# Kernel optimization log

Measured on AMD Instinct MI355X. Metric: run time of the kernel, lower is better.

The kernel has to match this reference:

```python
import jax, jax.numpy as jnp
import numpy as np

T, B, E, H = 200, 2048, 256, 512
P0, P1, NC = 256, 128, 1
ALPHA = 0.3  # keras LeakyReLU default


def _predict(h, W0, b0, W1, b1, Wf, bf):
    # Dense -> LeakyReLU -> (dropout=identity) x2, then sigmoid(Dense)
    h = jax.nn.leaky_relu(h @ W0 + b0, ALPHA)
    h = jax.nn.leaky_relu(h @ W1 + b1, ALPHA)
    return jax.nn.sigmoid(h @ Wf + bf)  # [B, 1]


def setup_inputs() -> dict:
    key = jax.random.key(0)
    ks = jax.random.split(key, 24)
    s = 0.05  # keras 'random_normal' initializer stddev
    d = {
        "inputs": jax.random.normal(ks[0], (T, B, E), jnp.float32),
        # gate order along leading axis: f, i, o, g
        "Wx_c": s * jax.random.normal(ks[1], (4, E, H), jnp.float32),
        "bx_c": jnp.zeros((4, H), jnp.float32),
        "Wh_c": s * jax.random.normal(ks[2], (4, H, H), jnp.float32),
        "Wx_v": s * jax.random.normal(ks[3], (4, E, H), jnp.float32),
        "bx_v": jnp.zeros((4, H), jnp.float32),
        "Wh_v": s * jax.random.normal(ks[4], (4, H, H), jnp.float32),
        # order: s_c_hat_c, s_c_hat_v, s_v_hat_v, s_v_hat_c
        "Ws": s * jax.random.normal(ks[5], (4, H, H), jnp.float32),
        "Wpc0": s * jax.random.normal(ks[6], (H, P0), jnp.float32),
        "bpc0": jnp.zeros((P0,), jnp.float32),
        "Wpc1": s * jax.random.normal(ks[7], (P0, P1), jnp.float32),
        "bpc1": jnp.zeros((P1,), jnp.float32),
        "Wfcc": s * jax.random.normal(ks[8], (P1, NC), jnp.float32),
        "bfcc": jnp.zeros((NC,), jnp.float32),
        "Wpv0": s * jax.random.normal(ks[9], (H, P0), jnp.float32),
        "bpv0": jnp.zeros((P0,), jnp.float32),
        "Wpv1": s * jax.random.normal(ks[10], (P0, P1), jnp.float32),
        "bpv1": jnp.zeros((P1,), jnp.float32),
        "Wfcv": s * jax.random.normal(ks[11], (P1, NC), jnp.float32),
        "bfcv": jnp.zeros((NC,), jnp.float32),
    }
    return d


def reference(inputs, Wx_c, bx_c, Wh_c, Wx_v, bx_v, Wh_v, Ws,
              Wpc0, bpc0, Wpc1, bpc1, Wfcc, bfcc,
              Wpv0, bpv0, Wpv1, bpv1, Wfcv, bfcv):
    batch = inputs.shape[1]
    zeros = jnp.zeros((batch, H), inputs.dtype)
    # initial g = predict_c(H_c=0), broadcast in place of tf.tile(g,[1,n_hidden])
    g0 = _predict(zeros, Wpc0, bpc0, Wpc1, bpc1, Wfcc, bfcc)  # [B,1]
    ones1 = jnp.ones_like(g0)

    def step(carry, x):
        H_c, H_v, s_c, s_v, g, pc, pv = carry
        # click stream gates: f,i,o,g fused along leading axis
        gx = jnp.einsum('be,keh->kbh', x, Wx_c) + bx_c[:, None, :]
        gh = jnp.einsum('bh,khg->kbg', H_c, Wh_c)
        pre = gx + gh
        f_c, i_c, o_c = jax.nn.sigmoid(pre[0]), jax.nn.sigmoid(pre[1]), jax.nn.sigmoid(pre[2])
        g_c = jnp.tanh(pre[3])
        s_c_hat = jnp.tanh((1.0 - g) * (H_c @ Ws[0]) + g * (H_v @ Ws[1]))
        s_c = s_c_hat + i_c * g_c + (1.0 - g) * (f_c * s_c)
        H_c = o_c * jnp.tanh(s_c)
        H_c_p = _predict(H_c, Wpc0, bpc0, Wpc1, bpc1, Wfcc, bfcc)  # [B,1]
        # no click_label branch: g = H_c_p
        g = H_c_p
        pc = jnp.where(H_c_p >= 0.5, ones1, (1.0 - H_c_p) * pc)
        # conversion stream gates (driven by updated H_c)
        gxv = jnp.einsum('be,keh->kbh', x, Wx_v) + bx_v[:, None, :]
        ghv = jnp.einsum('bh,khg->kbg', H_c, Wh_v)
        prev = gxv + ghv
        f_v, i_v, o_v = jax.nn.sigmoid(prev[0]), jax.nn.sigmoid(prev[1]), jax.nn.sigmoid(prev[2])
        g_v = jnp.tanh(prev[3])
        s_v_hat = jnp.tanh(H_v @ Ws[2] + g * (H_c @ Ws[3]))
        s_v = s_v_hat + (1.0 - g) * s_v + g * (f_v * s_v + i_v * g_v)
        H_v = (1.0 - g) * H_v + g * (o_v * jnp.tanh(s_v))
        H_v_p = _predict(H_v, Wpv0, bpv0, Wpv1, bpv1, Wfcv, bfcv) * H_c_p
        pv = jnp.where(H_c_p >= 0.5, ones1, (1.0 - H_v_p) * pv)
        return (H_c, H_v, s_c, s_v, g, pc, pv), (H_c_p, H_v_p)

    carry0 = (zeros, zeros, zeros, zeros, g0, ones1, ones1)
    _, (pred_c, pred_v) = jax.lax.scan(step, carry0, inputs)
    return pred_c, pred_v  # each [T, B, 1]
```

## Files before the change

kernel.cpp:

```cpp
#include <hip/hip_runtime.h>
#include <cstdint>
#include <cstddef>

constexpr int T_STEPS = 200;
constexpr int BATCH   = 2048;
constexpr int E_DIM   = 256;
constexpr int H_DIM   = 512;
constexpr int P0_DIM  = 256;
constexpr int P1_DIM  = 128;
constexpr float ALPHA = 0.3f;

typedef __attribute__((ext_vector_type(8))) _Float16 f16x8;
typedef __attribute__((ext_vector_type(4))) float f32x4;

__device__ __forceinline__ float sigmoidf_(float x){ return 1.0f/(1.0f+expf(-x)); }

__device__ __forceinline__ unsigned short f2h(float f){
    union { _Float16 h; unsigned short u; } v;
    v.h = (_Float16)f;
    return v.u;
}

#define GLOAD16(gp, lp) __builtin_amdgcn_global_load_lds( \
    (const __attribute__((address_space(1))) unsigned int*)(gp), \
    (__attribute__((address_space(3))) unsigned int*)(lp), 16, 0, 0)

template<int ROWS>
__device__ __forceinline__ void stage64(const unsigned short* __restrict__ src, int ldk,
                                        char* ldsbase){
    constexpr int TOT = ROWS * 8;
    const int tid = threadIdx.x;
#pragma unroll
    for (int i = 0; i < TOT/256; ++i){
        const int gsl = i*256 + tid;
        const int r = gsl >> 3, s = gsl & 7;
        const int ksrc = ((s ^ (r & 7)) << 3);
        GLOAD16(src + (size_t)r*ldk + ksrc, ldsbase + gsl*16);
    }
}

__device__ __forceinline__ f16x8 ldsfragh(const char* ldsbase, int row, int kslot){
    return *(const f16x8*)(ldsbase + row*128 + ((kslot ^ (row & 7)) << 4));
}

__device__ __forceinline__ void mm_loop128h(
    const unsigned short* __restrict__ A, int lda,
    const unsigned short* __restrict__ B, int ldb,
    int K, f32x4 (&acc)[4][4], char* lds, int wr, int wc, int lr, int lq)
{
    stage64<128>(A, lda, lds);
    stage64<128>(B, ldb, lds + 16384);
    int cur = 0;
    for (int k0 = 0; k0 < K; k0 += 64){
        char* bufc = lds + cur*32768;
        if (k0 + 64 < K){
            char* bufn = lds + (cur^1)*32768;
            stage64<128>(A + k0 + 64, lda, bufn);
            stage64<128>(B + k0 + 64, ldb, bufn + 16384);
            asm volatile("s_waitcnt vmcnt(8)" ::: "memory");
        } else {
            asm volatile("s_waitcnt vmcnt(0)" ::: "memory");
        }
        __builtin_amdgcn_s_barrier();
        __builtin_amdgcn_sched_barrier(0);
        __builtin_amdgcn_s_setprio(1);
#pragma unroll
        for (int kk = 0; kk < 2; ++kk){
            f16x8 a[4], b[4];
#pragma unroll
            for (int m = 0; m < 4; ++m) a[m] = ldsfragh(bufc, wr*64 + m*16 + lr, kk*4 + lq);
#pragma unroll
            for (int n = 0; n < 4; ++n) b[n] = ldsfragh(bufc + 16384, wc*64 + n*16 + lr, kk*4 + lq);
#pragma unroll
            for (int m = 0; m < 4; ++m)
#pragma unroll
                for (int n = 0; n < 4; ++n)
                    acc[m][n] = __builtin_amdgcn_mfma_f32_16x16x32_f16(a[m], b[n], acc[m][n], 0,0,0);
        }
        __builtin_amdgcn_s_setprio(0);
        __builtin_amdgcn_sched_barrier(0);
        __builtin_amdgcn_s_barrier();
        cur ^= 1;
    }
}

__device__ __forceinline__ void gates_tile(
    int id,
    const unsigned short* __restrict__ Xh,
    const unsigned short* __restrict__ Hh,
    const unsigned short* __restrict__ WT,
    const float* __restrict__ bias, float* __restrict__ gates,
    char* lds, int wr, int wc, int lr, int lq)
{
    const int sw = ((id & 7) << 5) + (id >> 3);
    const int brow = (sw & 15) * 128;
    const int bcol = (sw >> 4) * 128;

    f32x4 acc[4][4];
#pragma unroll
    for (int m = 0; m < 4; ++m)
#pragma unroll
        for (int n = 0; n < 4; ++n){ f32x4 z = {0.f,0.f,0.f,0.f}; acc[m][n] = z; }

    mm_loop128h(Xh + (size_t)brow*E_DIM, E_DIM,
                WT + (size_t)bcol*768, 768,
                E_DIM, acc, lds, wr, wc, lr, lq);
    mm_loop128h(Hh + (size_t)brow*H_DIM, H_DIM,
                WT + (size_t)bcol*768 + E_DIM, 768,
                H_DIM, acc, lds, wr, wc, lr, lq);

    const int z = bcol >> 9;
    const int hbase = (bcol & 511) + wc*64;
    float* gz = gates + (size_t)z * BATCH * H_DIM;
#pragma unroll
    for (int m = 0; m < 4; ++m){
#pragma unroll
        for (int n = 0; n < 4; ++n){
            const int h = hbase + n*16 + lr;
            const float bs = bias[z*H_DIM + h];
#pragma unroll
            for (int r = 0; r < 4; ++r){
                const int b2 = brow + wr*64 + m*16 + lq*4 + r;
                float v = acc[m][n][r] + bs;
                v = (z < 3) ? sigmoidf_(v) : tanhf(v);
                gz[(size_t)b2 * H_DIM + h] = v;
            }
        }
    }
}

__device__ __forceinline__ void comb_tile(
    int jid,
    const unsigned short* __restrict__ A,
    const unsigned short* __restrict__ B,
    float* __restrict__ outp, char* lds, int wr, int wc, int lr, int lq)
{
    const int brow = (jid >> 2) * 128, bcol = (jid & 3) * 128;
    f32x4 acc[4][4];
#pragma unroll
    for (int m = 0; m < 4; ++m)
#pragma unroll
        for (int n = 0; n < 4; ++n){ f32x4 z = {0.f,0.f,0.f,0.f}; acc[m][n] = z; }

    mm_loop128h(A + (size_t)brow*H_DIM, H_DIM,
                B + (size_t)bcol*H_DIM, H_DIM,
                H_DIM, acc, lds, wr, wc, lr, lq);
#pragma unroll
    for (int m = 0; m < 4; ++m){
#pragma unroll
        for (int n = 0; n < 4; ++n){
            const int h = bcol + wc*64 + n*16 + lr;
#pragma unroll
            for (int r = 0; r < 4; ++r){
                const int b2 = brow + wr*64 + m*16 + lq*4 + r;
                outp[(size_t)b2 * H_DIM + h] = acc[m][n][r];
            }
        }
    }
}

__device__ __forceinline__ void predict_dev(
    int pblk, const unsigned short* __restrict__ Hh,
    const unsigned short* __restrict__ W0T, const float* __restrict__ b0,
    const unsigned short* __restrict__ W1T, const float* __restrict__ b1,
    const float* __restrict__ Wf, const float* __restrict__ bf_,
    float* gstate, const float* __restrict__ gmul, float* pred, char* lds)
{
    char*  ldsA = lds;
    char*  ldsB = lds + 4096;
    char*  ldsP = lds + 36864;
    float* sums = (float*)(lds + 53248);
    const int tid = threadIdx.x, lane = tid & 63, w = tid >> 6;
    const int lr = lane & 15, lq = lane >> 4;
    const int brow = pblk * 32;

    f32x4 acc0[2][4];
#pragma unroll
    for (int m = 0; m < 2; ++m)
#pragma unroll
        for (int n = 0; n < 4; ++n){ f32x4 z = {0.f,0.f,0.f,0.f}; acc0[m][n] = z; }

    for (int k0 = 0; k0 < H_DIM; k0 += 64){
        stage64<32>(Hh + (size_t)brow*H_DIM + k0, H_DIM, ldsA);
        stage64<256>(W0T + k0, H_DIM, ldsB);
        __syncthreads();
#pragma unroll
        for (int kk = 0; kk < 2; ++kk){
            f16x8 a[2], b[4];
#pragma unroll
            for (int m = 0; m < 2; ++m) a[m] = ldsfragh(ldsA, m*16 + lr, kk*4 + lq);
#pragma unroll
            for (int n = 0; n < 4; ++n) b[n] = ldsfragh(ldsB, w*64 + n*16 + lr, kk*4 + lq);
#pragma unroll
            for (int m = 0; m < 2; ++m)
#pragma unroll
                for (int n = 0; n < 4; ++n)
                    acc0[m][n] = __builtin_amdgcn_mfma_f32_16x16x32_f16(a[m], b[n], acc0[m][n], 0,0,0);
        }
        __syncthreads();
    }
#pragma unroll
    for (int m = 0; m < 2; ++m){
#pragma unroll
        for (int n = 0; n < 4; ++n){
            const int col = w*64 + n*16 + lr;
            const float bs = b0[col];
#pragma unroll
            for (int r = 0; r < 4; ++r){
                const int row = m*16 + lq*4 + r;
                float x = acc0[m][n][r] + bs;
                x = (x > 0.0f) ? x : ALPHA*x;
                *(unsigned short*)(ldsP + row*512 + ((((col >> 3)) ^ (row & 7)) << 4) + (col & 7)*2) = f2h(x);
            }
        }
    }
    __syncthreads();

    f32x4 accp[2][2];
#pragma unroll
    for (int m = 0; m < 2; ++m)
#pragma unroll
        for (int n = 0; n < 2; ++n){ f32x4 z = {0.f,0.f,0.f,0.f}; accp[m][n] = z; }

    for (int k0 = 0; k0 < P0_DIM; k0 += 64){
        stage64<128>(W1T + k0, P0_DIM, ldsB);
        __syncthreads();
#pragma unroll
        for (int kk = 0; kk < 2; ++kk){
            f16x8 a[2], b[2];
#pragma unroll
            for (int m = 0; m < 2; ++m){
                const int row = m*16 + lr;
                const int slot = (k0 >> 3) + kk*4 + lq;
                a[m] = *(const f16x8*)(ldsP + row*512 + ((slot ^ (row & 7)) << 4));
            }
#pragma unroll
            for (int n = 0; n < 2; ++n) b[n] = ldsfragh(ldsB, w*32 + n*16 + lr, kk*4 + lq);
#pragma unroll
            for (int m = 0; m < 2; ++m)
#pragma unroll
                for (int n = 0; n < 2; ++n)
                    accp[m][n] = __builtin_amdgcn_mfma_f32_16x16x32_f16(a[m], b[n], accp[m][n], 0,0,0);
        }
        __syncthreads();
    }

    float part[8];
#pragma unroll
    for (int j = 0; j < 8; ++j) part[j] = 0.0f;
#pragma unroll
    for (int m = 0; m < 2; ++m){
#pragma unroll
        for (int n = 0; n < 2; ++n){
            const int col = w*32 + n*16 + lr;
            const float bs = b1[col], wf = Wf[col];
#pragma unroll
            for (int r = 0; r < 4; ++r){
                float x = accp[m][n][r] + bs;
                x = (x > 0.0f) ? x : ALPHA*x;
                part[m*4 + r] += x * wf;
            }
        }
    }
#pragma unroll
    for (int mask = 1; mask < 16; mask <<= 1)
#pragma unroll
        for (int j = 0; j < 8; ++j) part[j] += __shfl_xor(part[j], mask);
    if (lr == 0){
#pragma unroll
        for (int j = 0; j < 8; ++j){
            const int row = (j >> 2)*16 + lq*4 + (j & 3);
            sums[w*32 + row] = part[j];
        }
    }
    __syncthreads();
    if (tid < 32){
        float tot = sums[tid] + sums[32 + tid] + sums[64 + tid] + sums[96 + tid] + bf_[0];
        float val = sigmoidf_(tot);
        const int rowg = brow + tid;
        if (gmul)   val *= gmul[rowg];
        if (gstate) gstate[rowg] = val;
        if (pred)   pred[rowg]   = val;
    }
}

__device__ __forceinline__ void xcvt_dev(int blk, const float* __restrict__ x,
                                         unsigned short* __restrict__ oh)
{
    const int tid = threadIdx.x;
#pragma unroll
    for (int j = 0; j < 4; ++j){
        const int t = blk*256 + tid + j*32768;
        float4 v = ((const float4*)x)[t];
        ushort4 h;
        h.x = f2h(v.x); h.y = f2h(v.y); h.z = f2h(v.z); h.w = f2h(v.w);
        ((ushort4*)oh)[t] = h;
    }
}

__global__ __launch_bounds__(256, 2) void k_mmA(
    const unsigned short* __restrict__ Xh,
    const unsigned short* __restrict__ Hc, const unsigned short* __restrict__ Hv,
    const unsigned short* __restrict__ WT,
    const float* __restrict__ bias, float* __restrict__ gates,
    const unsigned short* __restrict__ Ws0, float* __restrict__ a1,
    const unsigned short* __restrict__ Ws1, float* __restrict__ a2,
    const unsigned short* __restrict__ Ws2, float* __restrict__ a1v,
    const unsigned short* __restrict__ W0Tv, const float* __restrict__ b0v,
    const unsigned short* __restrict__ W1Tv, const float* __restrict__ b1v,
    const float* __restrict__ Wfv, const float* __restrict__ bfv,
    const float* __restrict__ g, float* __restrict__ predv)
{
    __shared__ __align__(16) char lds[65536];
    const int tid = threadIdx.x;
    const int lane = tid & 63, wid = tid >> 6;
    const int wr = wid >> 1, wc = wid & 1;
    const int lr = lane & 15, lq = lane >> 4;
    const int id = blockIdx.x;

    if (id < 256){
        gates_tile(id, Xh, Hc, WT, bias, gates, lds, wr, wc, lr, lq);
    } else if (id < 448){
        const int j = (id - 256) >> 6, jid = (id - 256) & 63;
        if (j == 0)      comb_tile(jid, Hc, Ws0, a1,  lds, wr, wc, lr, lq);
        else if (j == 1) comb_tile(jid, Hv, Ws1, a2,  lds, wr, wc, lr, lq);
        else             comb_tile(jid, Hv, Ws2, a1v, lds, wr, wc, lr, lq);
    } else {
        predict_dev(id - 448, Hv, W0Tv, b0v, W1Tv, b1v, Wfv, bfv,
                    nullptr, g, predv, lds);
    }
}

__global__ __launch_bounds__(256, 2) void k_mmB(
    const unsigned short* __restrict__ Xh,
    const unsigned short* __restrict__ Hc,
    const unsigned short* __restrict__ WT,
    const float* __restrict__ bias, float* __restrict__ gates,
    const unsigned short* __restrict__ Ws3, float* __restrict__ a2v,
    const unsigned short* __restrict__ W0Tc, const float* __restrict__ b0c,
    const unsigned short* __restrict__ W1Tc, const float* __restrict__ b1c,
    const float* __restrict__ Wfc, const float* __restrict__ bfc,
    float* __restrict__ g, float* __restrict__ predc,
    const float* __restrict__ xnext, unsigned short* __restrict__ Xnh)
{
    __shared__ __align__(16) char lds[65536];
    const int tid = threadIdx.x;
    const int lane = tid & 63, wid = tid >> 6;
    const int wr = wid >> 1, wc = wid & 1;
    const int lr = lane & 15, lq = lane >> 4;
    const int id = blockIdx.x;

    if (id < 256){
        gates_tile(id, Xh, Hc, WT, bias, gates, lds, wr, wc, lr, lq);
    } else if (id < 320){
        comb_tile(id - 256, Hc, Ws3, a2v, lds, wr, wc, lr, lq);
    } else if (id < 384){
        predict_dev(id - 320, Hc, W0Tc, b0c, W1Tc, b1c, Wfc, bfc,
                    g, nullptr, predc, lds);
    } else {
        xcvt_dev(id - 384, xnext, Xnh);
    }
}

__global__ __launch_bounds__(256) void k_cell(
    const int mode, const float* __restrict__ gates, const float* __restrict__ a1,
    const float* __restrict__ a2, const float* __restrict__ g,
    float* __restrict__ sstate, float* __restrict__ Hv32,
    unsigned short* __restrict__ Outh)
{
    const size_t BH = (size_t)BATCH * H_DIM;
    const int i4 = blockIdx.x*256 + threadIdx.x;
    const size_t base = (size_t)i4 * 4;
    const int row = (int)(base >> 9);
    const float gv = g[row];
    union U4 { float4 v; float s[4]; };
    U4 f_, i_, o_, q_, u1, u2, sv, hv;
    f_.v = *(const float4*)&gates[base];
    i_.v = *(const float4*)&gates[BH + base];
    o_.v = *(const float4*)&gates[2*BH + base];
    q_.v = *(const float4*)&gates[3*BH + base];
    u1.v = *(const float4*)&a1[base];
    u2.v = *(const float4*)&a2[base];
    sv.v = *(const float4*)&sstate[base];
    if (mode == 1) hv.v = *(const float4*)&Hv32[base];
    U4 sn, hnew;
    union { unsigned short u[4]; ushort4 v; } hh;
#pragma unroll
    for (int e = 0; e < 4; ++e){
        float hval, s;
        if (mode == 0){
            const float shat = tanhf((1.0f - gv)*u1.s[e] + gv*u2.s[e]);
            s = shat + i_.s[e]*q_.s[e] + (1.0f - gv)*(f_.s[e]*sv.s[e]);
            hval = o_.s[e] * tanhf(s);
        } else {
            const float shat = tanhf(u1.s[e] + gv*u2.s[e]);
            const float svo = sv.s[e];
            s = shat + (1.0f - gv)*svo + gv*(f_.s[e]*svo + i_.s[e]*q_.s[e]);
            hval = (1.0f - gv)*hv.s[e] + gv*(o_.s[e]*tanhf(s));
            hnew.s[e] = hval;
        }
        sn.s[e] = s;
        hh.u[e] = f2h(hval);
    }
    *(float4*)&sstate[base] = sn.v;
    if (mode == 1) *(float4*)&Hv32[base] = hnew.v;
    *(ushort4*)&Outh[base] = hh.v;
}

__global__ __launch_bounds__(256) void k_predict_g(
    const unsigned short* __restrict__ Hh,
    const unsigned short* __restrict__ W0T, const float* __restrict__ b0,
    const unsigned short* __restrict__ W1T, const float* __restrict__ b1,
    const float* __restrict__ Wf, const float* __restrict__ bf_,
    float* gstate, const float* __restrict__ gmul, float* pred)
{
    __shared__ __align__(16) char lds[53760];
    predict_dev(blockIdx.x, Hh, W0T, b0, W1T, b1, Wf, bf_, gstate, gmul, pred, lds);
}

__global__ __launch_bounds__(256) void k_xcvt_g(const float* __restrict__ x,
                                                unsigned short* __restrict__ oh)
{
    xcvt_dev(blockIdx.x, x, oh);
}

__global__ __launch_bounds__(256) void k_wcat(const float* __restrict__ Wx,
                                              const float* __restrict__ Wh,
                                              unsigned short* __restrict__ oh){
    const int n = blockIdx.y;
    const int k = blockIdx.x*256 + threadIdx.x;
    const int z = n >> 9, h = n & 511;
    float v = (k < 256) ? Wx[((size_t)z*E_DIM + k)*H_DIM + h]
                        : Wh[((size_t)z*H_DIM + (k - 256))*H_DIM + h];
    oh[(size_t)n*768 + k] = f2h(v);
}

__global__ __launch_bounds__(256) void k_trans(const float* __restrict__ in,
                                               unsigned short* __restrict__ oh,
                                               int K, int N){
    const int k = blockIdx.x*256 + threadIdx.x;
    const int n = blockIdx.y;
    if (k < K) oh[(size_t)n*K + k] = f2h(in[(size_t)k*N + n]);
}

__global__ __launch_bounds__(256) void k_init(float* __restrict__ sc, float* __restrict__ sv,
                                              float* __restrict__ hv32,
                                              unsigned short* __restrict__ hc0,
                                              unsigned short* __restrict__ hv0){
    const int i = blockIdx.x*256 + threadIdx.x;
    sc[i] = 0.0f; sv[i] = 0.0f; hv32[i] = 0.0f;
    hc0[i] = 0; hv0[i] = 0;
}

extern "C" void kernel_launch(void* const* d_in, const int* in_sizes, int n_in,
                              void* d_out, int out_size, void* d_ws, size_t ws_size,
                              hipStream_t stream)
{
    (void)in_sizes; (void)n_in; (void)out_size; (void)ws_size;

    const float* inputs = (const float*)d_in[0];
    const float* Wx_c   = (const float*)d_in[1];
    const float* bx_c   = (const float*)d_in[2];
    const float* Wh_c   = (const float*)d_in[3];
    const float* Wx_v   = (const float*)d_in[4];
    const float* bx_v   = (const float*)d_in[5];
    const float* Wh_v   = (const float*)d_in[6];
    const float* Ws     = (const float*)d_in[7];
    const float* Wpc0   = (const float*)d_in[8];
    const float* bpc0   = (const float*)d_in[9];
    const float* Wpc1   = (const float*)d_in[10];
    const float* bpc1   = (const float*)d_in[11];
    const float* Wfcc   = (const float*)d_in[12];
    const float* bfcc   = (const float*)d_in[13];
    const float* Wpv0   = (const float*)d_in[14];
    const float* bpv0   = (const float*)d_in[15];
    const float* Wpv1   = (const float*)d_in[16];
    const float* bpv1   = (const float*)d_in[17];
    const float* Wfcv   = (const float*)d_in[18];
    const float* bfcv   = (const float*)d_in[19];
    float* out = (float*)d_out;

    char* ws = (char*)d_ws;
    size_t off = 0;
    auto allocB = [&](size_t bytes) -> char* {
        char* p = ws + off;
        off = (off + bytes + 255) & ~(size_t)255;
        return p;
    };
    const size_t BH = (size_t)BATCH * H_DIM;
    const size_t BE = (size_t)BATCH * E_DIM;

    unsigned short* Xh[2];
    Xh[0] = (unsigned short*)allocB(BE*2);
    Xh[1] = (unsigned short*)allocB(BE*2);
    unsigned short* WcTc  = (unsigned short*)allocB((size_t)2048*768*2);
    unsigned short* WcTv  = (unsigned short*)allocB((size_t)2048*768*2);
    unsigned short* WsT   = (unsigned short*)allocB((size_t)4*H_DIM*H_DIM*2);
    unsigned short* Wp0Tc = (unsigned short*)allocB((size_t)P0_DIM*H_DIM*2);
    unsigned short* Wp0Tv = (unsigned short*)allocB((size_t)P0_DIM*H_DIM*2);
    unsigned short* Wp1Tc = (unsigned short*)allocB((size_t)P1_DIM*P0_DIM*2);
    unsigned short* Wp1Tv = (unsigned short*)allocB((size_t)P1_DIM*P0_DIM*2);
    unsigned short* Hc    = (unsigned short*)allocB(BH*2);
    unsigned short* Hv    = (unsigned short*)allocB(BH*2);
    float* sc    = (float*)allocB(BH*4);
    float* sv    = (float*)allocB(BH*4);
    float* hv32  = (float*)allocB(BH*4);
    float* gates = (float*)allocB(4*BH*4);
    float* a1    = (float*)allocB(BH*4);
    float* a2    = (float*)allocB(BH*4);
    float* a1v   = (float*)allocB(BH*4);
    float* a2v   = (float*)allocB(BH*4);
    float* g     = (float*)allocB(BATCH*4);

    const dim3 thr(256);
    const size_t HH = (size_t)H_DIM * H_DIM;

    k_wcat<<<dim3(3, 2048), thr, 0, stream>>>(Wx_c, Wh_c, WcTc);
    k_wcat<<<dim3(3, 2048), thr, 0, stream>>>(Wx_v, Wh_v, WcTv);
    for (int i = 0; i < 4; ++i)
        k_trans<<<dim3(2, 512), thr, 0, stream>>>(Ws + i*HH, WsT + i*HH, H_DIM, H_DIM);
    k_trans<<<dim3(2, 256), thr, 0, stream>>>(Wpc0, Wp0Tc, H_DIM, P0_DIM);
    k_trans<<<dim3(2, 256), thr, 0, stream>>>(Wpv0, Wp0Tv, H_DIM, P0_DIM);
    k_trans<<<dim3(1, 128), thr, 0, stream>>>(Wpc1, Wp1Tc, P0_DIM, P1_DIM);
    k_trans<<<dim3(1, 128), thr, 0, stream>>>(Wpv1, Wp1Tv, P0_DIM, P1_DIM);

    k_init<<<4096, thr, 0, stream>>>(sc, sv, hv32, Hc, Hv);
    k_predict_g<<<64, thr, 0, stream>>>(Hc, Wp0Tc, bpc0, Wp1Tc, bpc1, Wfcc, bfcc,
                                        g, nullptr, nullptr);
    k_xcvt_g<<<128, thr, 0, stream>>>(inputs, Xh[0]);

    for (int t = 0; t < T_STEPS; ++t){
        const int xs = t & 1, xn = xs ^ 1;

        const int gridA = (t > 0) ? 512 : 448;
        k_mmA<<<gridA, thr, 0, stream>>>(Xh[xs], Hc, Hv,
                                         WcTc, bx_c, gates,
                                         WsT + 0*HH, a1,
                                         WsT + 1*HH, a2,
                                         WsT + 2*HH, a1v,
                                         Wp0Tv, bpv0, Wp1Tv, bpv1, Wfcv, bfcv,
                                         g, out + (size_t)(T_STEPS + t - 1)*BATCH);
        k_cell<<<1024, thr, 0, stream>>>(0, gates, a1, a2, g, sc, nullptr, Hc);

        const int gridB = (t + 1 < T_STEPS) ? 512 : 384;
        k_mmB<<<gridB, thr, 0, stream>>>(Xh[xs], Hc,
                                         WcTv, bx_v, gates,
                                         WsT + 3*HH, a2v,
                                         Wp0Tc, bpc0, Wp1Tc, bpc1, Wfcc, bfcc,
                                         g, out + (size_t)t*BATCH,
                                         inputs + (size_t)(t+1)*BE, Xh[xn]);
        k_cell<<<1024, thr, 0, stream>>>(1, gates, a1v, a2v, g, sv, hv32, Hv);
    }
    k_predict_g<<<64, thr, 0, stream>>>(Hv, Wp0Tv, bpv0, Wp1Tv, bpv1, Wfcv, bfcv,
                                        nullptr, g, out + (size_t)(2*T_STEPS - 1)*BATCH);
}
```

Baseline: 12.02 ms.

## Fuse gate GEMMs, Ws combos and cell update into one per-stream kernel

Replaces the separate gate GEMM, Ws combination GEMMs and elementwise cell kernels with a single fused kernel. Each block computes all four gates for a 64-row by 32-hidden slice together with both Ws projections, then applies the cell update straight from LDS. Weights are reordered so that one tile holds every gate for the same hidden units, and the H and g buffers are double-buffered. This removes the large fp32 round-trips for gates and a1/a2 and cuts launches per step from four to three. The trade-offs are a smaller MMA tile (64x128) with lower reuse, and moving the predictor and input conversion into a separate launch.

```diff
diff --git a/kernel.cpp b/kernel.cpp
--- a/kernel.cpp
+++ b/kernel.cpp
@@ -43,21 +43,31 @@
     return *(const f16x8*)(ldsbase + row*128 + ((kslot ^ (row & 7)) << 4));
 }
 
-__device__ __forceinline__ void mm_loop128h(
+template<bool HAS_B1, bool HAS_B2, int KSLABS>
+__device__ __forceinline__ void fused_phase(
     const unsigned short* __restrict__ A, int lda,
-    const unsigned short* __restrict__ B, int ldb,
-    int K, f32x4 (&acc)[4][4], char* lds, int wr, int wc, int lr, int lq)
-{
-    stage64<128>(A, lda, lds);
-    stage64<128>(B, ldb, lds + 16384);
+    const unsigned short* __restrict__ B1,
+    const unsigned short* __restrict__ B2,
+    f32x4 (&accg)[2][4], f32x4 (&acce)[2],
+    char* lds, int wr, int wc, int lr, int lq)
+{
+    stage64<64>(A, lda, lds);
+    if (HAS_B1) stage64<128>(B1, 768, lds + 8192);
+    if (HAS_B2) stage64<32>(B2, 512, lds + 24576);
     int cur = 0;
-    for (int k0 = 0; k0 < K; k0 += 64){
+    for (int s = 0; s < KSLABS; ++s){
         char* bufc = lds + cur*32768;
-        if (k0 + 64 < K){
+        if (s + 1 < KSLABS){
             char* bufn = lds + (cur^1)*32768;
-            stage64<128>(A + k0 + 64, lda, bufn);
-            stage64<128>(B + k0 + 64, ldb, bufn + 16384);
-            asm volatile("s_waitcnt vmcnt(8)" ::: "memory");
+            stage64<64>(A + (s+1)*64, lda, bufn);
+            if (HAS_B1) stage64<128>(B1 + (s+1)*64, 768, bufn + 8192);
+            if (HAS_B2) stage64<32>(B2 + (s+1)*64, 512, bufn + 24576);
+            if constexpr (HAS_B1 && HAS_B2)
+                asm volatile("s_waitcnt vmcnt(7)" ::: "memory");
+            else if constexpr (HAS_B1)
+                asm volatile("s_waitcnt vmcnt(6)" ::: "memory");
+            else
+                asm volatile("s_waitcnt vmcnt(3)" ::: "memory");
         } else {
             asm volatile("s_waitcnt vmcnt(0)" ::: "memory");
         }
@@ -66,16 +76,24 @@
         __builtin_amdgcn_s_setprio(1);
 #pragma unroll
         for (int kk = 0; kk < 2; ++kk){
-            f16x8 a[4], b[4];
-#pragma unroll
-            for (int m = 0; m < 4; ++m) a[m] = ldsfragh(bufc, wr*64 + m*16 + lr, kk*4 + lq);
-#pragma unroll
-            for (int n = 0; n < 4; ++n) b[n] = ldsfragh(bufc + 16384, wc*64 + n*16 + lr, kk*4 + lq);
-#pragma unroll
-            for (int m = 0; m < 4; ++m)
-#pragma unroll
-                for (int n = 0; n < 4; ++n)
-                    acc[m][n] = __builtin_amdgcn_mfma_f32_16x16x32_f16(a[m], b[n], acc[m][n], 0,0,0);
+            f16x8 a[2];
+#pragma unroll
+            for (int m = 0; m < 2; ++m) a[m] = ldsfragh(bufc, wr*32 + m*16 + lr, kk*4 + lq);
+            if (HAS_B1){
+#pragma unroll
+                for (int n = 0; n < 4; ++n){
+                    f16x8 b = ldsfragh(bufc + 8192, wc*64 + n*16 + lr, kk*4 + lq);
+#pragma unroll
+                    for (int m = 0; m < 2; ++m)
+                        accg[m][n] = __builtin_amdgcn_mfma_f32_16x16x32_f16(a[m], b, accg[m][n], 0,0,0);
+                }
+            }
+            if (HAS_B2){
+                f16x8 b = ldsfragh(bufc + 24576, wc*16 + lr, kk*4 + lq);
+#pragma unroll
+                for (int m = 0; m < 2; ++m)
+                    acce[m] = __builtin_amdgcn_mfma_f32_16x16x32_f16(a[m], b, acce[m], 0,0,0);
+            }
         }
         __builtin_amdgcn_s_setprio(0);
         __builtin_amdgcn_sched_barrier(0);
@@ -84,79 +102,129 @@
     }
 }
 
-__device__ __forceinline__ void gates_tile(
-    int id,
+__global__ __launch_bounds__(256, 2) void k_fused(
     const unsigned short* __restrict__ Xh,
-    const unsigned short* __restrict__ Hh,
-    const unsigned short* __restrict__ WT,
-    const float* __restrict__ bias, float* __restrict__ gates,
-    char* lds, int wr, int wc, int lr, int lq)
-{
-    const int sw = ((id & 7) << 5) + (id >> 3);
-    const int brow = (sw & 15) * 128;
-    const int bcol = (sw >> 4) * 128;
-
-    f32x4 acc[4][4];
-#pragma unroll
-    for (int m = 0; m < 4; ++m)
-#pragma unroll
-        for (int n = 0; n < 4; ++n){ f32x4 z = {0.f,0.f,0.f,0.f}; acc[m][n] = z; }
-
-    mm_loop128h(Xh + (size_t)brow*E_DIM, E_DIM,
-                WT + (size_t)bcol*768, 768,
-                E_DIM, acc, lds, wr, wc, lr, lq);
-    mm_loop128h(Hh + (size_t)brow*H_DIM, H_DIM,
-                WT + (size_t)bcol*768 + E_DIM, 768,
-                H_DIM, acc, lds, wr, wc, lr, lq);
-
-    const int z = bcol >> 9;
-    const int hbase = (bcol & 511) + wc*64;
-    float* gz = gates + (size_t)z * BATCH * H_DIM;
-#pragma unroll
-    for (int m = 0; m < 4; ++m){
+    const unsigned short* __restrict__ AH,
+    const unsigned short* __restrict__ AV,
+    const unsigned short* __restrict__ WT2,
+    const float* __restrict__ bias,
+    const unsigned short* __restrict__ WsH,
+    const unsigned short* __restrict__ WsV,
+    const float* __restrict__ g,
+    float* __restrict__ sstate, float* __restrict__ Hv32,
+    unsigned short* __restrict__ Hnew,
+    const int mode)
+{
+    __shared__ __align__(16) char lds[65536];
+    const int tid = threadIdx.x;
+    const int lane = tid & 63, wid = tid >> 6;
+    const int wr = wid >> 1, wc = wid & 1;
+    const int lr = lane & 15, lq = lane >> 4;
+
+    const int id = blockIdx.x;
+    const int virt = ((id & 7) << 6) | (id >> 3);
+    const int hgrp = virt >> 5;
+    const int brow = (virt & 31) * 64;
+    const int h0   = hgrp * 32;
+
+    f32x4 accg[2][4], acceH[2], acceV[2];
+#pragma unroll
+    for (int m = 0; m < 2; ++m){
+        f32x4 z = {0.f,0.f,0.f,0.f};
+#pragma unroll
+        for (int n = 0; n < 4; ++n) accg[m][n] = z;
+        acceH[m] = z; acceV[m] = z;
+    }
+
+    const unsigned short* WTp = WT2 + (size_t)hgrp*128*768;
+    fused_phase<true,false,4>(Xh + (size_t)brow*E_DIM, E_DIM, WTp, nullptr,
+                              accg, acceH, lds, wr, wc, lr, lq);
+    fused_phase<true,true,8>(AH + (size_t)brow*H_DIM, H_DIM, WTp + E_DIM,
+                             WsH + (size_t)h0*H_DIM,
+                             accg, acceH, lds, wr, wc, lr, lq);
+    fused_phase<false,true,8>(AV + (size_t)brow*H_DIM, H_DIM, nullptr,
+                              WsV + (size_t)h0*H_DIM,
+                              accg, acceV, lds, wr, wc, lr, lq);
+
+    float* ldsG  = (float*)lds;
+    float* ldsEH = (float*)(lds + 33792);
+    float* ldsEV = (float*)(lds + 42240);
+#pragma unroll
+    for (int m = 0; m < 2; ++m){
 #pragma unroll
         for (int n = 0; n < 4; ++n){
-            const int h = hbase + n*16 + lr;
-            const float bs = bias[z*H_DIM + h];
+            const int col = wc*64 + n*16 + lr;
+            const int z = col >> 5, hl = col & 31;
+            const float bs = bias[z*H_DIM + h0 + hl];
 #pragma unroll
             for (int r = 0; r < 4; ++r){
-                const int b2 = brow + wr*64 + m*16 + lq*4 + r;
-                float v = acc[m][n][r] + bs;
+                const int row = wr*32 + m*16 + lq*4 + r;
+                float v = accg[m][n][r] + bs;
                 v = (z < 3) ? sigmoidf_(v) : tanhf(v);
-                gz[(size_t)b2 * H_DIM + h] = v;
+                ldsG[row*132 + col] = v;
             }
         }
     }
-}
-
-__device__ __forceinline__ void comb_tile(
-    int jid,
-    const unsigned short* __restrict__ A,
-    const unsigned short* __restrict__ B,
-    float* __restrict__ outp, char* lds, int wr, int wc, int lr, int lq)
-{
-    const int brow = (jid >> 2) * 128, bcol = (jid & 3) * 128;
-    f32x4 acc[4][4];
-#pragma unroll
-    for (int m = 0; m < 4; ++m)
-#pragma unroll
-        for (int n = 0; n < 4; ++n){ f32x4 z = {0.f,0.f,0.f,0.f}; acc[m][n] = z; }
-
-    mm_loop128h(A + (size_t)brow*H_DIM, H_DIM,
-                B + (size_t)bcol*H_DIM, H_DIM,
-                H_DIM, acc, lds, wr, wc, lr, lq);
-#pragma unroll
-    for (int m = 0; m < 4; ++m){
-#pragma unroll
-        for (int n = 0; n < 4; ++n){
-            const int h = bcol + wc*64 + n*16 + lr;
-#pragma unroll
-            for (int r = 0; r < 4; ++r){
-                const int b2 = brow + wr*64 + m*16 + lq*4 + r;
-                outp[(size_t)b2 * H_DIM + h] = acc[m][n][r];
-            }
-        }
-    }
+#pragma unroll
+    for (int m = 0; m < 2; ++m){
+        const int col = wc*16 + lr;
+#pragma unroll
+        for (int r = 0; r < 4; ++r){
+            const int row = wr*32 + m*16 + lq*4 + r;
+            ldsEH[row*33 + col] = acceH[m][r];
+            ldsEV[row*33 + col] = acceV[m][r];
+        }
+    }
+    __syncthreads();
+
+    const int crow = tid >> 2, ch = (tid & 3) * 8;
+    const int grow = brow + crow;
+    const float gv = g[grow];
+    const size_t gbase = (size_t)grow*H_DIM + h0 + ch;
+    union U4 { float4 v; float s[4]; };
+    U4 sv0, sv1, hv0, hv1;
+    sv0.v = *(const float4*)&sstate[gbase];
+    sv1.v = *(const float4*)&sstate[gbase + 4];
+    if (mode == 1){
+        hv0.v = *(const float4*)&Hv32[gbase];
+        hv1.v = *(const float4*)&Hv32[gbase + 4];
+    }
+    U4 sn0, sn1, hn0, hn1;
+    union { unsigned short u[8]; f16x8 v; } hh;
+#pragma unroll
+    for (int e = 0; e < 8; ++e){
+        const int hc = ch + e;
+        const float f_ = ldsG[crow*132 + hc];
+        const float i_ = ldsG[crow*132 + 32 + hc];
+        const float o_ = ldsG[crow*132 + 64 + hc];
+        const float q_ = ldsG[crow*132 + 96 + hc];
+        const float eh = ldsEH[crow*33 + hc];
+        const float ev = ldsEV[crow*33 + hc];
+        const float a1 = (mode == 0) ? eh : ev;
+        const float a2 = (mode == 0) ? ev : eh;
+        const float svo = (e < 4) ? sv0.s[e] : sv1.s[e-4];
+        float s, hval;
+        if (mode == 0){
+            const float shat = tanhf((1.0f - gv)*a1 + gv*a2);
+            s = shat + i_*q_ + (1.0f - gv)*(f_*svo);
+            hval = o_ * tanhf(s);
+        } else {
+            const float shat = tanhf(a1 + gv*a2);
+            s = shat + (1.0f - gv)*svo + gv*(f_*svo + i_*q_);
+            const float hvo = (e < 4) ? hv0.s[e] : hv1.s[e-4];
+            hval = (1.0f - gv)*hvo + gv*(o_*tanhf(s));
+            if (e < 4) hn0.s[e] = hval; else hn1.s[e-4] = hval;
+        }
+        if (e < 4) sn0.s[e] = s; else sn1.s[e-4] = s;
+        hh.u[e] = f2h(hval);
+    }
+    *(float4*)&sstate[gbase]     = sn0.v;
+    *(float4*)&sstate[gbase + 4] = sn1.v;
+    if (mode == 1){
+        *(float4*)&Hv32[gbase]     = hn0.v;
+        *(float4*)&Hv32[gbase + 4] = hn1.v;
+    }
+    *(f16x8*)&Hnew[gbase] = hh.v;
 }
 
 __device__ __forceinline__ void predict_dev(
@@ -298,113 +366,30 @@
     }
 }
 
-__global__ __launch_bounds__(256, 2) void k_mmA(
-    const unsigned short* __restrict__ Xh,
-    const unsigned short* __restrict__ Hc, const unsigned short* __restrict__ Hv,
-    const unsigned short* __restrict__ WT,
-    const float* __restrict__ bias, float* __restrict__ gates,
-    const unsigned short* __restrict__ Ws0, float* __restrict__ a1,
-    const unsigned short* __restrict__ Ws1, float* __restrict__ a2,
-    const unsigned short* __restrict__ Ws2, float* __restrict__ a1v,
-    const unsigned short* __restrict__ W0Tv, const float* __restrict__ b0v,
-    const unsigned short* __restrict__ W1Tv, const float* __restrict__ b1v,
-    const float* __restrict__ Wfv, const float* __restrict__ bfv,
-    const float* __restrict__ g, float* __restrict__ predv)
-{
-    __shared__ __align__(16) char lds[65536];
-    const int tid = threadIdx.x;
-    const int lane = tid & 63, wid = tid >> 6;
-    const int wr = wid >> 1, wc = wid & 1;
-    const int lr = lane & 15, lq = lane >> 4;
+__global__ __launch_bounds__(256) void k_LB(
+    const unsigned short* __restrict__ Hcn,
+    const unsigned short* __restrict__ Wp0Tc, const float* __restrict__ bpc0,
+    const unsigned short* __restrict__ Wp1Tc, const float* __restrict__ bpc1,
+    const float* __restrict__ Wfcc, const float* __restrict__ bfcc,
+    float* __restrict__ gnew, float* __restrict__ predc,
+    const unsigned short* __restrict__ Hvb,
+    const unsigned short* __restrict__ Wp0Tv, const float* __restrict__ bpv0,
+    const unsigned short* __restrict__ Wp1Tv, const float* __restrict__ bpv1,
+    const float* __restrict__ Wfcv, const float* __restrict__ bfcv,
+    const float* __restrict__ gold, float* __restrict__ predv,
+    const float* __restrict__ xnext, unsigned short* __restrict__ Xnh)
+{
+    __shared__ __align__(16) char lds[53760];
     const int id = blockIdx.x;
-
-    if (id < 256){
-        gates_tile(id, Xh, Hc, WT, bias, gates, lds, wr, wc, lr, lq);
-    } else if (id < 448){
-        const int j = (id - 256) >> 6, jid = (id - 256) & 63;
-        if (j == 0)      comb_tile(jid, Hc, Ws0, a1,  lds, wr, wc, lr, lq);
-        else if (j == 1) comb_tile(jid, Hv, Ws1, a2,  lds, wr, wc, lr, lq);
-        else             comb_tile(jid, Hv, Ws2, a1v, lds, wr, wc, lr, lq);
+    if (id < 64){
+        predict_dev(id, Hcn, Wp0Tc, bpc0, Wp1Tc, bpc1, Wfcc, bfcc,
+                    gnew, nullptr, predc, lds);
+    } else if (id < 128){
+        if (predv) predict_dev(id - 64, Hvb, Wp0Tv, bpv0, Wp1Tv, bpv1, Wfcv, bfcv,
+                               nullptr, gold, predv, lds);
     } else {
-        predict_dev(id - 448, Hv, W0Tv, b0v, W1Tv, b1v, Wfv, bfv,
-                    nullptr, g, predv, lds);
-    }
-}
-
-__global__ __launch_bounds__(256, 2) void k_mmB(
-    const unsigned short* __restrict__ Xh,
-    const unsigned short* __restrict__ Hc,
-    const unsigned short* __restrict__ WT,
-    const float* __restrict__ bias, float* __restrict__ gates,
-    const unsigned short* __restrict__ Ws3, float* __restrict__ a2v,
-    const unsigned short* __restrict__ W0Tc, const float* __restrict__ b0c,
-    const unsigned short* __restrict__ W1Tc, const float* __restrict__ b1c,
-    const float* __restrict__ Wfc, const float* __restrict__ bfc,
-    float* __restrict__ g, float* __restrict__ predc,
-    const float* __restrict__ xnext, unsigned short* __restrict__ Xnh)
-{
-    __shared__ __align__(16) char lds[65536];
-    const int tid = threadIdx.x;
-    const int lane = tid & 63, wid = tid >> 6;
-    const int wr = wid >> 1, wc = wid & 1;
-    const int lr = lane & 15, lq = lane >> 4;
-    const int id = blockIdx.x;
-
-    if (id < 256){
-        gates_tile(id, Xh, Hc, WT, bias, gates, lds, wr, wc, lr, lq);
-    } else if (id < 320){
-        comb_tile(id - 256, Hc, Ws3, a2v, lds, wr, wc, lr, lq);
-    } else if (id < 384){
-        predict_dev(id - 320, Hc, W0Tc, b0c, W1Tc, b1c, Wfc, bfc,
-                    g, nullptr, predc, lds);
-    } else {
-        xcvt_dev(id - 384, xnext, Xnh);
-    }
-}
-
-__global__ __launch_bounds__(256) void k_cell(
-    const int mode, const float* __restrict__ gates, const float* __restrict__ a1,
-    const float* __restrict__ a2, const float* __restrict__ g,
-    float* __restrict__ sstate, float* __restrict__ Hv32,
-    unsigned short* __restrict__ Outh)
-{
-    const size_t BH = (size_t)BATCH * H_DIM;
-    const int i4 = blockIdx.x*256 + threadIdx.x;
-    const size_t base = (size_t)i4 * 4;
-    const int row = (int)(base >> 9);
-    const float gv = g[row];
-    union U4 { float4 v; float s[4]; };
-    U4 f_, i_, o_, q_, u1, u2, sv, hv;
-    f_.v = *(const float4*)&gates[base];
-    i_.v = *(const float4*)&gates[BH + base];
-    o_.v = *(const float4*)&gates[2*BH + base];
-    q_.v = *(const float4*)&gates[3*BH + base];
-    u1.v = *(const float4*)&a1[base];
-    u2.v = *(const float4*)&a2[base];
-    sv.v = *(const float4*)&sstate[base];
-    if (mode == 1) hv.v = *(const float4*)&Hv32[base];
-    U4 sn, hnew;
-    union { unsigned short u[4]; ushort4 v; } hh;
-#pragma unroll
-    for (int e = 0; e < 4; ++e){
-        float hval, s;
-        if (mode == 0){
-            const float shat = tanhf((1.0f - gv)*u1.s[e] + gv*u2.s[e]);
-            s = shat + i_.s[e]*q_.s[e] + (1.0f - gv)*(f_.s[e]*sv.s[e]);
-            hval = o_.s[e] * tanhf(s);
-        } else {
-            const float shat = tanhf(u1.s[e] + gv*u2.s[e]);
-            const float svo = sv.s[e];
-            s = shat + (1.0f - gv)*svo + gv*(f_.s[e]*svo + i_.s[e]*q_.s[e]);
-            hval = (1.0f - gv)*hv.s[e] + gv*(o_.s[e]*tanhf(s));
-            hnew.s[e] = hval;
-        }
-        sn.s[e] = s;
-        hh.u[e] = f2h(hval);
-    }
-    *(float4*)&sstate[base] = sn.v;
-    if (mode == 1) *(float4*)&Hv32[base] = hnew.v;
-    *(ushort4*)&Outh[base] = hh.v;
+        if (Xnh) xcvt_dev(id - 128, xnext, Xnh);
+    }
 }
 
 __global__ __launch_bounds__(256) void k_predict_g(
@@ -429,7 +414,8 @@
                                               unsigned short* __restrict__ oh){
     const int n = blockIdx.y;
     const int k = blockIdx.x*256 + threadIdx.x;
-    const int z = n >> 9, h = n & 511;
+    const int z = (n >> 5) & 3;
+    const int h = ((n >> 7) << 5) | (n & 31);
     float v = (k < 256) ? Wx[((size_t)z*E_DIM + k)*H_DIM + h]
                         : Wh[((size_t)z*H_DIM + (k - 256))*H_DIM + h];
     oh[(size_t)n*768 + k] = f2h(v);
@@ -493,30 +479,30 @@
     unsigned short* Xh[2];
     Xh[0] = (unsigned short*)allocB(BE*2);
     Xh[1] = (unsigned short*)allocB(BE*2);
-    unsigned short* WcTc  = (unsigned short*)allocB((size_t)2048*768*2);
-    unsigned short* WcTv  = (unsigned short*)allocB((size_t)2048*768*2);
+    unsigned short* WT2c  = (unsigned short*)allocB((size_t)2048*768*2);
+    unsigned short* WT2v  = (unsigned short*)allocB((size_t)2048*768*2);
     unsigned short* WsT   = (unsigned short*)allocB((size_t)4*H_DIM*H_DIM*2);
     unsigned short* Wp0Tc = (unsigned short*)allocB((size_t)P0_DIM*H_DIM*2);
     unsigned short* Wp0Tv = (unsigned short*)allocB((size_t)P0_DIM*H_DIM*2);
     unsigned short* Wp1Tc = (unsigned short*)allocB((size_t)P1_DIM*P0_DIM*2);
     unsigned short* Wp1Tv = (unsigned short*)allocB((size_t)P1_DIM*P0_DIM*2);
-    unsigned short* Hc    = (unsigned short*)allocB(BH*2);
-    unsigned short* Hv    = (unsigned short*)allocB(BH*2);
+    unsigned short* Hc[2], *Hv[2];
+    Hc[0] = (unsigned short*)allocB(BH*2);
+    Hc[1] = (unsigned short*)allocB(BH*2);
+    Hv[0] = (unsigned short*)allocB(BH*2);
+    Hv[1] = (unsigned short*)allocB(BH*2);
     float* sc    = (float*)allocB(BH*4);
     float* sv    = (float*)allocB(BH*4);
     float* hv32  = (float*)allocB(BH*4);
-    float* gates = (float*)allocB(4*BH*4);
-    float* a1    = (float*)allocB(BH*4);
-    float* a2    = (float*)allocB(BH*4);
-    float* a1v   = (float*)allocB(BH*4);
-    float* a2v   = (float*)allocB(BH*4);
-    float* g     = (float*)allocB(BATCH*4);
+    float* gbuf[2];
+    gbuf[0] = (float*)allocB(BATCH*4);
+    gbuf[1] = (float*)allocB(BATCH*4);
 
     const dim3 thr(256);
     const size_t HH = (size_t)H_DIM * H_DIM;
 
-    k_wcat<<<dim3(3, 2048), thr, 0, stream>>>(Wx_c, Wh_c, WcTc);
-    k_wcat<<<dim3(3, 2048), thr, 0, stream>>>(Wx_v, Wh_v, WcTv);
+    k_wcat<<<dim3(3, 2048), thr, 0, stream>>>(Wx_c, Wh_c, WT2c);
+    k_wcat<<<dim3(3, 2048), thr, 0, stream>>>(Wx_v, Wh_v, WT2v);
     for (int i = 0; i < 4; ++i)
         k_trans<<<dim3(2, 512), thr, 0, stream>>>(Ws + i*HH, WsT + i*HH, H_DIM, H_DIM);
     k_trans<<<dim3(2, 256), thr, 0, stream>>>(Wpc0, Wp0Tc, H_DIM, P0_DIM);
@@ -524,33 +510,36 @@
     k_trans<<<dim3(1, 128), thr, 0, stream>>>(Wpc1, Wp1Tc, P0_DIM, P1_DIM);
     k_trans<<<dim3(1, 128), thr, 0, stream>>>(Wpv1, Wp1Tv, P0_DIM, P1_DIM);
 
-    k_init<<<4096, thr, 0, stream>>>(sc, sv, hv32, Hc, Hv);
-    k_predict_g<<<64, thr, 0, stream>>>(Hc, Wp0Tc, bpc0, Wp1Tc, bpc1, Wfcc, bfcc,
-                                        g, nullptr, nullptr);
+    k_init<<<4096, thr, 0, stream>>>(sc, sv, hv32, Hc[0], Hv[0]);
+    k_predict_g<<<64, thr, 0, stream>>>(Hc[0], Wp0Tc, bpc0, Wp1Tc, bpc1, Wfcc, bfcc,
+                                        gbuf[0], nullptr, nullptr);
     k_xcvt_g<<<128, thr, 0, stream>>>(inputs, Xh[0]);
 
     for (int t = 0; t < T_STEPS; ++t){
-        const int xs = t & 1, xn = xs ^ 1;
-
-        const int gridA = (t > 0) ? 512 : 448;
-        k_mmA<<<gridA, thr, 0, stream>>>(Xh[xs], Hc, Hv,
-                                         WcTc, bx_c, gates,
-                                         WsT + 0*HH, a1,
-                                         WsT + 1*HH, a2,
-                                         WsT + 2*HH, a1v,
-                                         Wp0Tv, bpv0, Wp1Tv, bpv1, Wfcv, bfcv,
-                                         g, out + (size_t)(T_STEPS + t - 1)*BATCH);
-        k_cell<<<1024, thr, 0, stream>>>(0, gates, a1, a2, g, sc, nullptr, Hc);
-
-        const int gridB = (t + 1 < T_STEPS) ? 512 : 384;
-        k_mmB<<<gridB, thr, 0, stream>>>(Xh[xs], Hc,
-                                         WcTv, bx_v, gates,
-                                         WsT + 3*HH, a2v,
-                                         Wp0Tc, bpc0, Wp1Tc, bpc1, Wfcc, bfcc,
-                                         g, out + (size_t)t*BATCH,
-                                         inputs + (size_t)(t+1)*BE, Xh[xn]);
-        k_cell<<<1024, thr, 0, stream>>>(1, gates, a1v, a2v, g, sv, hv32, Hv);
-    }
-    k_predict_g<<<64, thr, 0, stream>>>(Hv, Wp0Tv, bpv0, Wp1Tv, bpv1, Wfcv, bfcv,
-                                        nullptr, g, out + (size_t)(2*T_STEPS - 1)*BATCH);
-}
+        const int cur = t & 1, nxt = cur ^ 1;
+
+        k_fused<<<512, thr, 0, stream>>>(Xh[cur], Hc[cur], Hv[cur],
+                                         WT2c, bx_c,
+                                         WsT + 0*HH,
+                                         WsT + 1*HH,
+                                         gbuf[cur], sc, nullptr, Hc[nxt], 0);
+
+        k_LB<<<256, thr, 0, stream>>>(Hc[nxt], Wp0Tc, bpc0, Wp1Tc, bpc1, Wfcc, bfcc,
+                                      gbuf[nxt], out + (size_t)t*BATCH,
+                                      Hv[cur], Wp0Tv, bpv0, Wp1Tv, bpv1, Wfcv, bfcv,
+                                      gbuf[cur],
+                                      (t > 0) ? out + (size_t)(T_STEPS + t - 1)*BATCH
+                                              : nullptr,
+                                      inputs + (size_t)(t+1)*BE,
+                                      (t + 1 < T_STEPS) ? Xh[nxt] : nullptr);
+
+        k_fused<<<512, thr, 0, stream>>>(Xh[cur], Hc[nxt], Hv[cur],
+                                         WT2v, bx_v,
+                                         WsT + 3*HH,
+                                         WsT + 2*HH,
+                                         gbuf[nxt], sv, hv32, Hv[nxt], 1);
+    }
+    k_predict_g<<<64, thr, 0, stream>>>(Hv[0], Wp0Tv, bpv0, Wp1Tv, bpv1, Wfcv, bfcv,
+                                        nullptr, gbuf[0],
+                                        out + (size_t)(2*T_STEPS - 1)*BATCH);
+}
```

Result: faster. 10.47 ms (median of 2 runs) (-12.9%).
